# Kernel optimization log

Hardware: AMD Instinct MI355X
Metric: run time of the kernel (lower is better)

Reference implementation:

```python
import jax, jax.numpy as jnp
import numpy as np

NCONF, NT, NX = 8192, 64, 64


def setup_inputs() -> dict:
    key = jax.random.key(0)
    k1, k2, k3 = jax.random.split(key, 3)
    phi = jax.random.normal(k1, (NCONF, NT, NX), dtype=jnp.float32)
    # Well-conditioned invertible mixing matrix so logdet is finite/stable.
    W = jnp.eye(NX, dtype=jnp.float32) + 0.1 * jax.random.normal(k2, (NX, NX), dtype=jnp.float32)
    b = 0.1 * jax.random.normal(k3, (NX,), dtype=jnp.float32)
    return {"phi": phi, "W": W, "b": b}


def _nn(phi, W, b):
    # Wrapped NN: invertible linear coupling along the Nx axis.
    NNphi = jnp.einsum('btx,xy->bty', phi, W) + b
    _, logabsdet = jnp.linalg.slogdet(W)
    logDet = jnp.full((phi.shape[0],), phi.shape[1] * logabsdet, dtype=phi.dtype)
    return NNphi, logDet


def reference(phi, W, b):
    Nconf, Nt, Nx = phi.shape
    # t[i, x] = argmin over time of |phi[i, :, x]|  -> [Nconf, Nx]
    t = jnp.argmin(jnp.abs(phi), axis=1)
    # Source: if t[i,0] > t[i,1]: T0[i] = t[i,1]; config.flip(1) is DISCARDED (no-op).
    T0 = jnp.where(t[:, 0] > t[:, 1], t[:, 1], t[:, 0])  # [Nconf]
    j = jnp.arange(Nx)
    # torch.roll(x, s, dim): out[j] = x[(j - s) % N]
    idx_fwd = (j[None, :] - T0[:, None]) % Nx          # [Nconf, Nx]
    phi_r = jnp.take_along_axis(phi, idx_fwd[:, None, :], axis=2)
    NNphi, logDet = _nn(phi_r, W, b)
    # roll back with shift -T0; flip again discarded in source.
    idx_bwd = (j[None, :] + T0[:, None]) % Nx
    NNphi = jnp.take_along_axis(NNphi, idx_bwd[:, None, :], axis=2)
    return NNphi, logDet
```

## Files before the change

### kernel.cpp

```cpp
#include <hip/hip_runtime.h>
#include <stdint.h>


typedef _Float16 half8v __attribute__((ext_vector_type(8)));
typedef _Float16 half4v __attribute__((ext_vector_type(4)));
typedef float float4v __attribute__((ext_vector_type(4)));

__device__ __forceinline__ float rdlane_f(float v, int l) {
  return __int_as_float(__builtin_amdgcn_readlane(__float_as_int(v), l));
}

__global__ __launch_bounds__(256) void wt2_prep(const float* __restrict__ W,
                                                _Float16* __restrict__ wt2) {
  const int s = blockIdx.x;
  const int tid = threadIdx.x;
#pragma unroll
  for (int it = 0; it < 16; ++it) {
    int flat = it * 256 + tid;
    int j = flat >> 6, y = flat & 63;
    wt2[(size_t)s * 4096 + flat] =
        (_Float16)W[((y + s) & 63) * 64 + ((j + s) & 63)];
  }
}

__global__ __launch_bounds__(256) void equiv_main(
    const float* __restrict__ phi, const float* __restrict__ W,
    const float* __restrict__ b, const _Float16* __restrict__ wt2,
    float* __restrict__ out) {
  __shared__ __align__(16) _Float16 smem[4][4096];
  const int lane = threadIdx.x & 63;
  const int wave = threadIdx.x >> 6;

  if (blockIdx.x == 0) {
    if (threadIdx.x >= 64) return;
    const int t = lane;
    float r[64];
#pragma unroll
    for (int i = 0; i < 64; ++i) r[i] = W[t * 64 + i];
    float ldsum = 0.f;
#pragma unroll 1
    for (int k = 0; k < 64; ++k) {
      float v0 = r[0];
      float piv = rdlane_f(v0, k);
      ldsum += logf(fabsf(piv));
      float mf = v0 / piv;
#pragma unroll
      for (int i = 1; i < 64; ++i) {
        float pe = rdlane_f(r[i], k);
        r[i - 1] = r[i] - mf * pe;
      }
      r[63] = 0.f;
    }
    float ld = 64.0f * ldsum;
    float* outLD = out + (size_t)8192 * 4096;
#pragma unroll
    for (int it = 0; it < 128; ++it) outLD[it * 64 + t] = ld;
    return;
  }

  const int cfg = ((int)blockIdx.x - 1) * 4 + wave;
  const int m = lane & 15;
  const int q = lane >> 4;

  const float* ph = phi + (size_t)cfg * 4096;
  float4v fr[16];
#pragma unroll
  for (int i = 0; i < 16; ++i) fr[i] = *(const float4v*)&ph[i * 256 + lane * 4];

  unsigned long long k0 = ~0ull, k1 = ~0ull;
  if (m == 0) {
#pragma unroll
    for (int i = 0; i < 16; ++i) {
      unsigned long long tt = (unsigned long long)(i * 4 + q);
      unsigned long long c0 =
          (((unsigned long long)__float_as_uint(fabsf(fr[i].x))) << 6) | tt;
      unsigned long long c1 =
          (((unsigned long long)__float_as_uint(fabsf(fr[i].y))) << 6) | tt;
      k0 = c0 < k0 ? c0 : k0;
      k1 = c1 < k1 ? c1 : k1;
    }
  }
#pragma unroll
  for (int s = 1; s < 64; s <<= 1) {
    unsigned long long o0 = __shfl_xor(k0, s);
    unsigned long long o1 = __shfl_xor(k1, s);
    k0 = o0 < k0 ? o0 : k0;
    k1 = o1 < k1 ? o1 : k1;
  }
  const int t0i = (int)(k0 & 63ull), t1i = (int)(k1 & 63ull);
  const int T0 = (t0i > t1i) ? t1i : t0i;

  const _Float16* wt = wt2 + (size_t)T0 * 4096;
  half8v Bf[2][4];
#pragma unroll
  for (int ks = 0; ks < 2; ++ks)
#pragma unroll
    for (int nt = 0; nt < 4; ++nt)
      Bf[ks][nt] = *(const half8v*)&wt[(nt * 16 + m) * 64 + ks * 32 + q * 8];
  float bias[4];
#pragma unroll
  for (int nt = 0; nt < 4; ++nt) bias[nt] = b[(nt * 16 + m + T0) & 63];

  _Float16* sw = smem[wave];
#pragma unroll
  for (int i = 0; i < 16; ++i) {
    int row = i * 4 + q;
    int dwc = (m * 2) ^ ((row & 7) << 2);
    half4v h;
    h[0] = (_Float16)fr[i][0];
    h[1] = (_Float16)fr[i][1];
    h[2] = (_Float16)fr[i][2];
    h[3] = (_Float16)fr[i][3];
    *(half4v*)&sw[row * 64 + dwc * 2] = h;
  }
  asm volatile("s_waitcnt lgkmcnt(0)" ::: "memory");
  __builtin_amdgcn_sched_barrier(0);

  half8v Af[4][2];
#pragma unroll
  for (int mt = 0; mt < 4; ++mt)
#pragma unroll
    for (int ks = 0; ks < 2; ++ks) {
      int row = mt * 16 + m;
      int dwc = (ks * 16 + q * 4) ^ ((row & 7) << 2);
      Af[mt][ks] = *(const half8v*)&sw[row * 64 + dwc * 2];
    }

  float4v acc[4][4];
#pragma unroll
  for (int mt = 0; mt < 4; ++mt)
#pragma unroll
    for (int nt = 0; nt < 4; ++nt) acc[mt][nt] = (float4v)(0.f);
#pragma unroll
  for (int ks = 0; ks < 2; ++ks)
#pragma unroll
    for (int mt = 0; mt < 4; ++mt)
#pragma unroll
      for (int nt = 0; nt < 4; ++nt)
        acc[mt][nt] = __builtin_amdgcn_mfma_f32_16x16x32_f16(
            Af[mt][ks], Bf[ks][nt], acc[mt][nt], 0, 0, 0);

  float* fsm = (float*)smem[wave];
  float* op = out + (size_t)cfg * 4096;
#pragma unroll
  for (int s = 0; s < 2; ++s) {
    asm volatile("s_waitcnt lgkmcnt(0)" ::: "memory");
    __builtin_amdgcn_sched_barrier(0);
#pragma unroll
    for (int mh = 0; mh < 2; ++mh) {
      int mt = s * 2 + mh;
#pragma unroll
      for (int nt = 0; nt < 4; ++nt)
#pragma unroll
        for (int r = 0; r < 4; ++r) {
          int lrow = mh * 16 + q * 4 + r;
          int dwc = (nt * 16 + m) ^ ((lrow & 7) << 2);
          fsm[lrow * 64 + dwc] = acc[mt][nt][r] + bias[nt];
        }
    }
    asm volatile("s_waitcnt lgkmcnt(0)" ::: "memory");
    __builtin_amdgcn_sched_barrier(0);
#pragma unroll
    for (int j = 0; j < 8; ++j) {
      int flat = j * 256 + lane * 4;
      int lrow = flat >> 6;
      int dwc = (flat & 63) ^ ((lrow & 7) << 2);
      float4v v = *(const float4v*)&fsm[lrow * 64 + dwc];
      __builtin_nontemporal_store(v, (float4v*)&op[s * 2048 + flat]);
    }
  }
}

extern "C" void kernel_launch(void* const* d_in, const int* in_sizes, int n_in,
                              void* d_out, int out_size, void* d_ws,
                              size_t ws_size, hipStream_t stream) {
  const float* phi = (const float*)d_in[0];
  const float* W = (const float*)d_in[1];
  const float* b = (const float*)d_in[2];
  float* out = (float*)d_out;
  _Float16* wt2 = (_Float16*)d_ws;

  wt2_prep<<<dim3(64), dim3(256), 0, stream>>>(W, wt2);
  equiv_main<<<dim3(2049), dim3(256), 0, stream>>>(phi, W, b, wt2, out);
}
```

Before: 242.9 us.

## Process four configs per wave with software-prefetched phi loads and double-buffered LDS

Each wave now handles four configurations in sequence. The next configuration's phi tile is loaded into registers while the current one is converted, multiplied with MFMA and stored, and LDS is double-buffered per wave. The grid shrinks to 1024 blocks of 128 threads. The logdet computation moves into a working block's first wave instead of a dedicated block. The LDS swizzle patterns also change. The aim is to hide global load latency behind compute, at the cost of doubled fragment registers, fewer resident waves, and serialising the logdet wave's first block.

```diff
diff --git a/kernel.cpp b/kernel.cpp
--- a/kernel.cpp
+++ b/kernel.cpp
@@ -23,16 +23,17 @@
   }
 }
 
-__global__ __launch_bounds__(256) void equiv_main(
+__global__ __launch_bounds__(128, 2) void equiv_main(
     const float* __restrict__ phi, const float* __restrict__ W,
     const float* __restrict__ b, const _Float16* __restrict__ wt2,
     float* __restrict__ out) {
-  __shared__ __align__(16) _Float16 smem[4][4096];
+  __shared__ __align__(16) _Float16 smem[2][2][4096];
   const int lane = threadIdx.x & 63;
   const int wave = threadIdx.x >> 6;
+  const int m = lane & 15;
+  const int q = lane >> 4;
 
-  if (blockIdx.x == 0) {
-    if (threadIdx.x >= 64) return;
+  if (blockIdx.x == 1 && wave == 0) {
     const int t = lane;
     float r[64];
 #pragma unroll
@@ -55,120 +56,126 @@
     float* outLD = out + (size_t)8192 * 4096;
 #pragma unroll
     for (int it = 0; it < 128; ++it) outLD[it * 64 + t] = ld;
-    return;
   }
 
-  const int cfg = ((int)blockIdx.x - 1) * 4 + wave;
-  const int m = lane & 15;
-  const int q = lane >> 4;
+  const int cfg0 = ((int)blockIdx.x * 2 + wave) * 4;
 
-  const float* ph = phi + (size_t)cfg * 4096;
-  float4v fr[16];
+  float4v frA[16], frB[16];
+
+  auto issue = [&](int k, float4v(&fr)[16]) {
+    const float* ph = phi + (size_t)(cfg0 + k) * 4096;
 #pragma unroll
-  for (int i = 0; i < 16; ++i) fr[i] = *(const float4v*)&ph[i * 256 + lane * 4];
+    for (int i = 0; i < 16; ++i)
+      fr[i] = *(const float4v*)&ph[i * 256 + lane * 4];
+  };
 
-  unsigned long long k0 = ~0ull, k1 = ~0ull;
-  if (m == 0) {
+  auto body = [&](int k, float4v(&fr)[16], float4v(&frn)[16]) {
+    _Float16* buf = smem[wave][k & 1];
+    unsigned long long k0 = ~0ull, k1 = ~0ull;
+    if (m == 0) {
+#pragma unroll
+      for (int i = 0; i < 16; ++i) {
+        unsigned long long tt = (unsigned long long)(i * 4 + q);
+        unsigned long long c0 =
+            (((unsigned long long)__float_as_uint(fabsf(fr[i].x))) << 6) | tt;
+        unsigned long long c1 =
+            (((unsigned long long)__float_as_uint(fabsf(fr[i].y))) << 6) | tt;
+        k0 = c0 < k0 ? c0 : k0;
+        k1 = c1 < k1 ? c1 : k1;
+      }
+    }
+#pragma unroll
+    for (int s = 1; s < 64; s <<= 1) {
+      unsigned long long o0 = __shfl_xor(k0, s);
+      unsigned long long o1 = __shfl_xor(k1, s);
+      k0 = o0 < k0 ? o0 : k0;
+      k1 = o1 < k1 ? o1 : k1;
+    }
+    const int t0i = (int)(k0 & 63ull), t1i = (int)(k1 & 63ull);
+    const int T0 = (t0i > t1i) ? t1i : t0i;
+
+    const _Float16* wt = wt2 + (size_t)T0 * 4096;
+    half8v Bf[2][4];
+#pragma unroll
+    for (int ks = 0; ks < 2; ++ks)
+#pragma unroll
+      for (int nt = 0; nt < 4; ++nt)
+        Bf[ks][nt] = *(const half8v*)&wt[(nt * 16 + m) * 64 + ks * 32 + q * 8];
+    float bias[4];
+#pragma unroll
+    for (int nt = 0; nt < 4; ++nt) bias[nt] = b[(nt * 16 + m + T0) & 63];
+    asm volatile("" ::: "memory");
+
 #pragma unroll
     for (int i = 0; i < 16; ++i) {
-      unsigned long long tt = (unsigned long long)(i * 4 + q);
-      unsigned long long c0 =
-          (((unsigned long long)__float_as_uint(fabsf(fr[i].x))) << 6) | tt;
-      unsigned long long c1 =
-          (((unsigned long long)__float_as_uint(fabsf(fr[i].y))) << 6) | tt;
-      k0 = c0 < k0 ? c0 : k0;
-      k1 = c1 < k1 ? c1 : k1;
-    }
-  }
-#pragma unroll
-  for (int s = 1; s < 64; s <<= 1) {
-    unsigned long long o0 = __shfl_xor(k0, s);
-    unsigned long long o1 = __shfl_xor(k1, s);
-    k0 = o0 < k0 ? o0 : k0;
-    k1 = o1 < k1 ? o1 : k1;
-  }
-  const int t0i = (int)(k0 & 63ull), t1i = (int)(k1 & 63ull);
-  const int T0 = (t0i > t1i) ? t1i : t0i;
-
-  const _Float16* wt = wt2 + (size_t)T0 * 4096;
-  half8v Bf[2][4];
-#pragma unroll
-  for (int ks = 0; ks < 2; ++ks)
-#pragma unroll
-    for (int nt = 0; nt < 4; ++nt)
-      Bf[ks][nt] = *(const half8v*)&wt[(nt * 16 + m) * 64 + ks * 32 + q * 8];
-  float bias[4];
-#pragma unroll
-  for (int nt = 0; nt < 4; ++nt) bias[nt] = b[(nt * 16 + m + T0) & 63];
-
-  _Float16* sw = smem[wave];
-#pragma unroll
-  for (int i = 0; i < 16; ++i) {
-    int row = i * 4 + q;
-    int dwc = (m * 2) ^ ((row & 7) << 2);
-    half4v h;
-    h[0] = (_Float16)fr[i][0];
-    h[1] = (_Float16)fr[i][1];
-    h[2] = (_Float16)fr[i][2];
-    h[3] = (_Float16)fr[i][3];
-    *(half4v*)&sw[row * 64 + dwc * 2] = h;
-  }
-  asm volatile("s_waitcnt lgkmcnt(0)" ::: "memory");
-  __builtin_amdgcn_sched_barrier(0);
-
-  half8v Af[4][2];
-#pragma unroll
-  for (int mt = 0; mt < 4; ++mt)
-#pragma unroll
-    for (int ks = 0; ks < 2; ++ks) {
-      int row = mt * 16 + m;
-      int dwc = (ks * 16 + q * 4) ^ ((row & 7) << 2);
-      Af[mt][ks] = *(const half8v*)&sw[row * 64 + dwc * 2];
+      int row = i * 4 + q;
+      half4v h;
+      h[0] = (_Float16)fr[i][0];
+      h[1] = (_Float16)fr[i][1];
+      h[2] = (_Float16)fr[i][2];
+      h[3] = (_Float16)fr[i][3];
+      *(half4v*)&buf[row * 64 + ((((m >> 1) ^ (row & 7)) << 3) | ((m & 1) << 2))] = h;
     }
 
-  float4v acc[4][4];
-#pragma unroll
-  for (int mt = 0; mt < 4; ++mt)
-#pragma unroll
-    for (int nt = 0; nt < 4; ++nt) acc[mt][nt] = (float4v)(0.f);
-#pragma unroll
-  for (int ks = 0; ks < 2; ++ks)
+    if (k < 3) issue(k + 1, frn);
+    asm volatile("" ::: "memory");
+
+    half8v Af[4][2];
 #pragma unroll
     for (int mt = 0; mt < 4; ++mt)
 #pragma unroll
-      for (int nt = 0; nt < 4; ++nt)
-        acc[mt][nt] = __builtin_amdgcn_mfma_f32_16x16x32_f16(
-            Af[mt][ks], Bf[ks][nt], acc[mt][nt], 0, 0, 0);
+      for (int ks = 0; ks < 2; ++ks) {
+        int row = mt * 16 + m;
+        Af[mt][ks] =
+            *(const half8v*)&buf[row * 64 + (((ks * 4 + q) ^ (row & 7)) << 3)];
+      }
 
-  float* fsm = (float*)smem[wave];
-  float* op = out + (size_t)cfg * 4096;
+    float4v acc[4][4];
 #pragma unroll
-  for (int s = 0; s < 2; ++s) {
-    asm volatile("s_waitcnt lgkmcnt(0)" ::: "memory");
-    __builtin_amdgcn_sched_barrier(0);
+    for (int mt = 0; mt < 4; ++mt)
 #pragma unroll
-    for (int mh = 0; mh < 2; ++mh) {
-      int mt = s * 2 + mh;
+      for (int nt = 0; nt < 4; ++nt) acc[mt][nt] = (float4v)(0.f);
 #pragma unroll
-      for (int nt = 0; nt < 4; ++nt)
+    for (int ks = 0; ks < 2; ++ks)
 #pragma unroll
-        for (int r = 0; r < 4; ++r) {
-          int lrow = mh * 16 + q * 4 + r;
-          int dwc = (nt * 16 + m) ^ ((lrow & 7) << 2);
-          fsm[lrow * 64 + dwc] = acc[mt][nt][r] + bias[nt];
-        }
+      for (int mt = 0; mt < 4; ++mt)
+#pragma unroll
+        for (int nt = 0; nt < 4; ++nt)
+          acc[mt][nt] = __builtin_amdgcn_mfma_f32_16x16x32_f16(
+              Af[mt][ks], Bf[ks][nt], acc[mt][nt], 0, 0, 0);
+
+    float* fsm = (float*)buf;
+    float* op = out + (size_t)(cfg0 + k) * 4096;
+#pragma unroll
+    for (int s = 0; s < 2; ++s) {
+#pragma unroll
+      for (int mh = 0; mh < 2; ++mh) {
+        int mt = s * 2 + mh;
+#pragma unroll
+        for (int nt = 0; nt < 4; ++nt)
+#pragma unroll
+          for (int r2 = 0; r2 < 4; ++r2) {
+            int lrow = mh * 16 + q * 4 + r2;
+            fsm[lrow * 64 + ((nt * 16 + m) ^ ((lrow & 12) << 1))] =
+                acc[mt][nt][r2] + bias[nt];
+          }
+      }
+#pragma unroll
+      for (int j = 0; j < 8; ++j) {
+        int flat = j * 256 + lane * 4;
+        int lrow = flat >> 6, colg = flat & 63;
+        float4v v = *(const float4v*)&fsm[lrow * 64 + (colg ^ ((lrow & 12) << 1))];
+        __builtin_nontemporal_store(v, (float4v*)&op[s * 2048 + flat]);
+      }
     }
-    asm volatile("s_waitcnt lgkmcnt(0)" ::: "memory");
-    __builtin_amdgcn_sched_barrier(0);
-#pragma unroll
-    for (int j = 0; j < 8; ++j) {
-      int flat = j * 256 + lane * 4;
-      int lrow = flat >> 6;
-      int dwc = (flat & 63) ^ ((lrow & 7) << 2);
-      float4v v = *(const float4v*)&fsm[lrow * 64 + dwc];
-      __builtin_nontemporal_store(v, (float4v*)&op[s * 2048 + flat]);
-    }
-  }
+  };
+
+  issue(0, frA);
+  asm volatile("" ::: "memory");
+  body(0, frA, frB);
+  body(1, frB, frA);
+  body(2, frA, frB);
+  body(3, frB, frA);
 }
 
 extern "C" void kernel_launch(void* const* d_in, const int* in_sizes, int n_in,
@@ -181,5 +188,5 @@
   _Float16* wt2 = (_Float16*)d_ws;
 
   wt2_prep<<<dim3(64), dim3(256), 0, stream>>>(W, wt2);
-  equiv_main<<<dim3(2049), dim3(256), 0, stream>>>(phi, W, b, wt2, out);
+  equiv_main<<<dim3(1024), dim3(128), 0, stream>>>(phi, W, b, wt2, out);
 }
```

Result: no change. 244.5 us (+0.7%).
